# Performance work log

Hardware: AMD Instinct MI355X
Metric: run time of the kernel (lower is better)

## Reference

```python
import jax, jax.numpy as jnp
import numpy as np

B, N, K = 8, 2048, 64
RADII = (0.1, 0.3, 0.7)
TU = 256   # t_net_units
U = 512    # mmtsc_units
BLK = [(512, 512), (512, 256), (256, 170)]  # pce_depth=3, filters U//(i+1)
EPS = 1e-3  # keras BatchNormalization epsilon
BN_SCALE = np.float32(1.0 / np.sqrt(1.0 + EPS))  # inference BN: mean=0, var=1


def bn(x, g, b):
    return x * (g * BN_SCALE) + b


def setup_inputs():
    key = jax.random.key(0)
    ks = jax.random.split(key, 32)
    r = lambda i, sh, s=0.1: jax.random.normal(ks[i], sh, dtype=jnp.float32) * s
    inp = {
        "points": jax.random.normal(ks[0], (B, N, 3), dtype=jnp.float32),
        "noise": jax.random.uniform(ks[1], (B, N, N), dtype=jnp.float32),
        "tw": r(2, (3, TU)), "tb": r(3, (TU,)),
        "tg1": 1.0 + r(4, (TU,)), "tbt1": r(5, (TU,)),
        "td1w": r(6, (TU, TU)), "td1b": r(7, (TU,)),
        "tg2": 1.0 + r(8, (TU,)), "tbt2": r(9, (TU,)),
        "td2w": r(10, (TU, 9), 0.01), "td2b": jnp.ones((9,), jnp.float32),
        "c1w": r(11, (3 * K * 3, U)), "c1b": r(12, (U,)),
        "g1": 1.0 + r(13, (U,)), "be1": r(14, (U,)),
        "rw": r(15, (U, U)), "rb": r(16, (U,)),
    }
    for i, (ci, co) in enumerate(BLK):
        j = 17 + 4 * i
        inp[f"b{i+1}w"] = r(j, (ci, co))
        inp[f"b{i+1}b"] = r(j + 1, (co,))
        inp[f"b{i+1}g"] = 1.0 + r(j + 2, (co,))
        inp[f"b{i+1}be"] = r(j + 3, (co,))
    return inp


def reference(points, noise, tw, tb, tg1, tbt1, td1w, td1b, tg2, tbt2, td2w, td2b,
              c1w, c1b, g1, be1, rw, rb,
              b1w, b1b, b1g, b1be, b2w, b2b, b2g, b2be, b3w, b3b, b3g, b3be):
    relu = jax.nn.relu
    # ---- T-Net (dropout inactive at inference) ----
    x = relu(bn(points @ tw + tb, tg1, tbt1))       # [B,N,TU] (1x1 conv)
    x = jnp.max(x, axis=1)                          # GlobalMaxPooling1D -> [B,TU]
    x = relu(bn(x @ td1w + td1b, tg2, tbt2))        # [B,TU]
    T = (x @ td2w + td2b).reshape(-1, 3, 3)         # [B,3,3]
    pts = points @ T                                # [B,N,3]
    # ---- pairwise distances + multi-scale ball query ----
    diff = pts[:, :, None, :] - pts[:, None, :, :]  # [B,N,N,3]
    d = jax.lax.stop_gradient(jnp.sqrt(jnp.sum(diff * diff, axis=-1)))  # [B,N,N]
    bidx = jnp.arange(B)[:, None, None]
    groups = []
    for rad in RADII:
        score = jnp.where(d <= rad, noise, 0.0)     # mask * uniform
        idx = jnp.argsort(-score, axis=-1)[:, :, :K]  # descending, top-K  [B,N,K]
        groups.append(pts[bidx, idx])               # gather -> [B,N,K,3]
    feats = jnp.concatenate(groups, axis=-1).reshape(B, N, 3 * K * 3)  # [B,N,576]
    # ---- MLP stack (1x1 convs) ----
    f = relu(bn(feats @ c1w + c1b, g1, be1))        # [B,N,U]
    f = f + (f @ rw + rb)                           # residual
    for w, b_, g, be in ((b1w, b1b, b1g, b1be), (b2w, b2b, b2g, b2be), (b3w, b3b, b3g, b3be)):
        f = relu(bn(f @ w + b_, g, be))
    return jnp.max(f, axis=1)                       # [B,170]
```

## Files before the change

### kernel.cpp

```cpp
#include <hip/hip_runtime.h>
#include <hip/hip_bf16.h>


#define BN_SCALE 0.99950037468777f

typedef short short8 __attribute__((ext_vector_type(8)));
typedef float floatx4 __attribute__((ext_vector_type(4)));

typedef __attribute__((address_space(1))) const short gshort;
typedef __attribute__((address_space(3))) short lshort;

#define OFF_FEATS 0
#define OFF_R1    18874368
#define OFF_W     (OFF_R1 + 16777216)
#define OFF_C1WT  (OFF_W)
#define OFF_RWT   (OFF_C1WT + 589824)
#define OFF_B1WT  (OFF_RWT + 524288)
#define OFF_B2WT  (OFF_B1WT + 524288)
#define OFF_B3WT  (OFF_B2WT + 262144)
#define OFF_PTS   (OFF_B3WT + 131072)
#define OFF_PART  (OFF_PTS + 196608)

__device__ inline short f2bf(float x) {
    __hip_bfloat16 h = __float2bfloat16(x);
    return *reinterpret_cast<short*>(&h);
}
__device__ inline float bf2f(short s) {
    return __uint_as_float(((unsigned)(unsigned short)s) << 16);
}

__global__ __launch_bounds__(256)
void init_k(const float* __restrict__ c1w, const float* __restrict__ rw,
            const float* __restrict__ b1w, const float* __restrict__ b2w,
            const float* __restrict__ b3w,
            short* __restrict__ c1wT, short* __restrict__ rwT,
            short* __restrict__ b1wT, short* __restrict__ b2wT,
            short* __restrict__ b3wT,
            const float* __restrict__ points, const float* __restrict__ tw,
            const float* __restrict__ tb, const float* __restrict__ tg1,
            const float* __restrict__ tbt1, float* __restrict__ part,
            float* __restrict__ outF, int out_n) {
    __shared__ float smem[64 * 65];
    const int bid = blockIdx.x;
    if (bid < 248) {
        float (*tile)[65] = (float(*)[65])smem;
        const float* src; short* dst; int K, N, t;
        if (bid < 72)       { src = c1w; dst = c1wT; K = 576; N = 512; t = bid; }
        else if (bid < 136) { src = rw;  dst = rwT;  K = 512; N = 512; t = bid - 72; }
        else if (bid < 200) { src = b1w; dst = b1wT; K = 512; N = 512; t = bid - 136; }
        else if (bid < 232) { src = b2w; dst = b2wT; K = 512; N = 256; t = bid - 200; }
        else                { src = b3w; dst = b3wT; K = 256; N = 170; t = bid - 232; }
        int ktiles = K >> 6;
        int k0 = (t % ktiles) * 64, n0 = (t / ktiles) * 64;
        int tx = threadIdx.x & 63, ty = threadIdx.x >> 6;
#pragma unroll
        for (int p = 0; p < 16; p++) {
            int r = p * 4 + ty;
            int n = n0 + tx;
            tile[r][tx] = (n < N) ? src[(size_t)(k0 + r) * N + n] : 0.f;
        }
        __syncthreads();
#pragma unroll
        for (int p = 0; p < 16; p++) {
            int r = p * 4 + ty;
            dst[(size_t)(n0 + r) * K + k0 + tx] = f2bf(tile[tx][r]);
        }
    } else if (bid < 312) {
        float* spts = smem;
        const int t2 = bid - 248;
        const int chunk = t2 & 7, b = t2 >> 3;
        const int u = threadIdx.x;
        const float* pb = points + ((size_t)b * 2048 + chunk * 256) * 3;
        for (int i = u; i < 768; i += 256) spts[i] = pb[i];
        const float w0 = tw[u], w1 = tw[256 + u], w2 = tw[512 + u];
        const float bi = tb[u];
        const float gs = tg1[u] * BN_SCALE, bt = tbt1[u];
        __syncthreads();
        float m = 0.f;
        for (int nn = 0; nn < 256; nn++) {
            float v = spts[nn * 3] * w0 + spts[nn * 3 + 1] * w1 +
                      spts[nn * 3 + 2] * w2 + bi;
            v = fmaxf(v * gs + bt, 0.f);
            m = fmaxf(m, v);
        }
        part[((b * 8 + chunk) << 8) + u] = m;
    } else {
        for (int i = threadIdx.x; i < out_n; i += 256) outF[i] = 0.f;
    }
}

__global__ __launch_bounds__(1024)
void tnet2_k(const float* __restrict__ points, const float* __restrict__ part,
             const float* __restrict__ td1w, const float* __restrict__ td1b,
             const float* __restrict__ tg2, const float* __restrict__ tbt2,
             const float* __restrict__ td2w, const float* __restrict__ td2b,
             float* __restrict__ pts_out) {
    __shared__ float sx[256], sp[4][256], sx2[256], sp2[9][32], sT[9];
    const int b = blockIdx.x;
    const int tid = threadIdx.x;
    if (tid < 256) {
        float m = 0.f;
#pragma unroll
        for (int c = 0; c < 8; c++) m = fmaxf(m, part[((b * 8 + c) << 8) + tid]);
        sx[tid] = m;
    }
    __syncthreads();
    {
        int t = tid & 255, g = tid >> 8;
        float s = 0.f;
#pragma unroll 8
        for (int i = 0; i < 64; i++) {
            int v = g * 64 + i;
            s += sx[v] * td1w[v * 256 + t];
        }
        sp[g][t] = s;
    }
    __syncthreads();
    if (tid < 256) {
        float s = td1b[tid] + sp[0][tid] + sp[1][tid] + sp[2][tid] + sp[3][tid];
        sx2[tid] = fmaxf(s * (tg2[tid] * BN_SCALE) + tbt2[tid], 0.f);
    }
    __syncthreads();
    if (tid < 288) {
        int j = tid / 32, vg = tid & 31;
        float s = 0.f;
#pragma unroll
        for (int i = 0; i < 8; i++) {
            int v = vg * 8 + i;
            s += sx2[v] * td2w[v * 9 + j];
        }
        sp2[j][vg] = s;
    }
    __syncthreads();
    if (tid < 9) {
        float s = td2b[tid];
        for (int vg = 0; vg < 32; vg++) s += sp2[tid][vg];
        sT[tid] = s;
    }
    __syncthreads();
    for (int n = tid; n < 2048; n += 1024) {
        size_t idx = ((size_t)b * 2048 + n) * 3;
        float p0 = points[idx], p1 = points[idx + 1], p2 = points[idx + 2];
        pts_out[idx]     = p0 * sT[0] + p1 * sT[3] + p2 * sT[6];
        pts_out[idx + 1] = p0 * sT[1] + p1 * sT[4] + p2 * sT[7];
        pts_out[idx + 2] = p0 * sT[2] + p1 * sT[5] + p2 * sT[8];
    }
}

__device__ inline unsigned dpp_shr1(unsigned v) {
    return (unsigned)__builtin_amdgcn_update_dpp(0, (int)v, 0x138 ,
                                                 0xF, 0xF, false);
}

__device__ inline void ins_one(unsigned& llo, unsigned& lhi, unsigned vlo,
                               unsigned vhi, int lane) {
    unsigned long long lv = ((unsigned long long)lhi << 32) | llo;
    unsigned long long vv = ((unsigned long long)vhi << 32) | vlo;
    unsigned long long ltm = __ballot(lv < vv);
    if (ltm) {
        int p = __builtin_ctzll(ltm);
        unsigned uplo = dpp_shr1(llo);
        unsigned uphi = dpp_shr1(lhi);
        if (lane >= p) {
            llo = (lane == p) ? vlo : uplo;
            lhi = (lane == p) ? vhi : uphi;
        }
    }
}

__device__ inline void run_q(unsigned& llo, unsigned& lhi, unsigned long long& th,
                             unsigned klo, unsigned khi, unsigned long long qual,
                             int lane) {
    do {
        int src = __builtin_ctzll(qual);
        qual &= qual - 1;
        unsigned vlo = (unsigned)__builtin_amdgcn_readlane((int)klo, src);
        unsigned vhi = (unsigned)__builtin_amdgcn_readlane((int)khi, src);
        ins_one(llo, lhi, vlo, vhi, lane);
    } while (qual);
    th = ((unsigned long long)(unsigned)__builtin_amdgcn_readlane((int)lhi, 63) << 32)
         | (unsigned)__builtin_amdgcn_readlane((int)llo, 63);
}

__device__ inline void init_radius(bool in, unsigned nb, unsigned klo, int lane,
                                   unsigned& llo, unsigned& lhi,
                                   unsigned long long& th) {
    unsigned long long inm = __ballot(in);
    int S = 64 - __builtin_popcountll(inm);
    int mbI = __builtin_amdgcn_mbcnt_hi((unsigned)(inm >> 32),
              __builtin_amdgcn_mbcnt_lo((unsigned)inm, 0));
    int mbS = lane - mbI;
    int dst = in ? (S + mbI) : mbS;
    llo = (unsigned)__builtin_amdgcn_ds_permute(dst << 2, in ? 0 : (int)klo);
    lhi = 0;
    if (inm) {
        do {
            int src = __builtin_ctzll(inm);
            inm &= inm - 1;
            unsigned vlo = (unsigned)__builtin_amdgcn_readlane((int)klo, src);
            unsigned vhi = (unsigned)__builtin_amdgcn_readlane((int)nb, src);
            ins_one(llo, lhi, vlo, vhi, lane);
        } while (inm);
    }
    th = ((unsigned long long)(unsigned)__builtin_amdgcn_readlane((int)lhi, 63) << 32)
         | (unsigned)__builtin_amdgcn_readlane((int)llo, 63);
}

__global__ __launch_bounds__(512)
void topk_feats_k(const float* __restrict__ pts, const float* __restrict__ noise,
                  short* __restrict__ feats) {
    __shared__ float sxp[2048], syp[2048], szp[2048];
    const int b = blockIdx.y;
    const int tid = threadIdx.x;
    const int lane = tid & 63;
    const int wave = tid >> 6;
    const int n = blockIdx.x * 8 + wave;
    const float* nrow = noise + ((size_t)b * 2048 + n) * 2048;
    float ncur = nrow[lane];
    float nnxt = nrow[64 + lane];
    for (int i = tid; i < 2048; i += 512) {
        size_t p = ((size_t)b * 2048 + i) * 3;
        sxp[i] = pts[p];
        syp[i] = pts[p + 1];
        szp[i] = pts[p + 2];
    }
    __syncthreads();
    const float qx = sxp[n], qy = syp[n], qz = szp[n];

    unsigned L0lo, L0hi, L1lo, L1hi, L2lo, L2hi;
    unsigned long long th0, th1, th2;
    {
        float dx = qx - sxp[lane], dy = qy - syp[lane], dz = qz - szp[lane];
        float d = sqrtf(dx * dx + dy * dy + dz * dz);
        unsigned nb = __float_as_uint(ncur);
        unsigned klo = 2047 - lane;
        init_radius(d <= 0.1f, nb, klo, lane, L0lo, L0hi, th0);
        init_radius(d <= 0.3f, nb, klo, lane, L1lo, L1hi, th1);
        init_radius(d <= 0.7f, nb, klo, lane, L2lo, L2hi, th2);
    }
    for (int base = 64; base < 2048; base += 64) {
        float cur = nnxt;
        if (base + 64 < 2048) nnxt = nrow[base + 64 + lane];
        const int j = base + lane;
        float dx = qx - sxp[j], dy = qy - syp[j], dz = qz - szp[j];
        float d = sqrtf(dx * dx + dy * dy + dz * dz);
        unsigned nb = __float_as_uint(cur);
        unsigned klo = 2047 - j;
        unsigned k0hi = (d <= 0.1f) ? nb : 0u;
        unsigned k1hi = (d <= 0.3f) ? nb : 0u;
        unsigned k2hi = (d <= 0.7f) ? nb : 0u;
        unsigned long long key0 = ((unsigned long long)k0hi << 32) | klo;
        unsigned long long key1 = ((unsigned long long)k1hi << 32) | klo;
        unsigned long long key2 = ((unsigned long long)k2hi << 32) | klo;
        unsigned long long q0 = __ballot(key0 > th0);
        unsigned long long q1 = __ballot(key1 > th1);
        unsigned long long q2 = __ballot(key2 > th2);
        if (q0) run_q(L0lo, L0hi, th0, klo, k0hi, q0, lane);
        if (q1) run_q(L1lo, L1hi, th1, klo, k1hi, q1, lane);
        if (q2) run_q(L2lo, L2hi, th2, klo, k2hi, q2, lane);
    }
    size_t basef = ((size_t)b * 2048 + n) * 576 + (size_t)lane * 9;
    int j0 = 2047 - (int)(L0lo & 0x7FFu);
    int j1 = 2047 - (int)(L1lo & 0x7FFu);
    int j2 = 2047 - (int)(L2lo & 0x7FFu);
    feats[basef + 0] = f2bf(sxp[j0]);
    feats[basef + 1] = f2bf(syp[j0]);
    feats[basef + 2] = f2bf(szp[j0]);
    feats[basef + 3] = f2bf(sxp[j1]);
    feats[basef + 4] = f2bf(syp[j1]);
    feats[basef + 5] = f2bf(szp[j1]);
    feats[basef + 6] = f2bf(sxp[j2]);
    feats[basef + 7] = f2bf(syp[j2]);
    feats[basef + 8] = f2bf(szp[j2]);
}

template <int EPI>
__global__ __launch_bounds__(256)
void gemm_k(const short* __restrict__ A, const short* __restrict__ BT,
            int K, int Nact,
            const float* __restrict__ bias, const float* __restrict__ gamma,
            const float* __restrict__ beta,
            short* __restrict__ outB, float* __restrict__ outF,
            const short* __restrict__ resid) {
    __shared__ short sA[2][128 * 32];
    __shared__ short sB[2][128 * 32];
    const int tid = threadIdx.x;
    const int lane = tid & 63;
    const int wave = tid >> 6;
    const int wm = wave & 1, wn = wave >> 1;
    const int lr = lane & 15, lq = lane >> 4;
    const long m0 = (long)blockIdx.x * 128;
    const long n0 = (long)blockIdx.y * 128;

    const int srow = (lane >> 2);
    const int sp8 = (lane & 3) * 8;

    auto stage = [&](int buf, int k0) {
#pragma unroll
        for (int c = 0; c < 2; c++) {
            int chunk = wave * 2 + c;
            int rr = chunk * 16 + srow;
            __builtin_amdgcn_global_load_lds(
                (gshort*)(A + (m0 + rr) * K + k0 + sp8),
                (lshort*)&sA[buf][chunk * 512], 16, 0, 0);
            __builtin_amdgcn_global_load_lds(
                (gshort*)(BT + (n0 + rr) * K + k0 + sp8),
                (lshort*)&sB[buf][chunk * 512], 16, 0, 0);
        }
    };

    floatx4 acc[4][4];
#pragma unroll
    for (int i = 0; i < 4; i++)
#pragma unroll
        for (int j = 0; j < 4; j++) acc[i][j] = (floatx4){0.f, 0.f, 0.f, 0.f};

    const int T = K >> 5;
    stage(0, 0);
    __syncthreads();
    int cur = 0;
    for (int t = 0; t < T; ++t) {
        if (t + 1 < T) stage(cur ^ 1, (t + 1) << 5);
        short8 af[4], bf[4];
#pragma unroll
        for (int i = 0; i < 4; i++)
            af[i] = *(const short8*)(&sA[cur][(wm * 64 + i * 16 + lr) * 32 + lq * 8]);
#pragma unroll
        for (int j = 0; j < 4; j++)
            bf[j] = *(const short8*)(&sB[cur][(wn * 64 + j * 16 + lr) * 32 + lq * 8]);
#pragma unroll
        for (int i = 0; i < 4; i++)
#pragma unroll
            for (int j = 0; j < 4; j++)
                acc[i][j] = __builtin_amdgcn_mfma_f32_16x16x32_bf16(af[i], bf[j],
                                                                    acc[i][j], 0, 0, 0);
        __syncthreads();
        cur ^= 1;
    }

#pragma unroll
    for (int j = 0; j < 4; j++) {
        long col = n0 + wn * 64 + j * 16 + lr;
        if (col >= Nact) continue;
        float bi = bias[col];
        float gs = 0.f, bt = 0.f;
        if (EPI != 1) { gs = gamma[col] * BN_SCALE; bt = beta[col]; }
        float colmax = 0.f;
#pragma unroll
        for (int i = 0; i < 4; i++) {
#pragma unroll
            for (int rg = 0; rg < 4; rg++) {
                long row = m0 + wm * 64 + i * 16 + lq * 4 + rg;
                float v = acc[i][j][rg];
                if (EPI == 1) {
                    v = v + bi + bf2f(resid[row * Nact + col]);
                    outB[row * Nact + col] = f2bf(v);
                } else {
                    v = fmaxf((v + bi) * gs + bt, 0.f);
                    if (EPI == 0) outB[row * Nact + col] = f2bf(v);
                    else colmax = fmaxf(colmax, v);
                }
            }
        }
        if (EPI == 2) {
            colmax = fmaxf(colmax, __shfl_xor(colmax, 16));
            colmax = fmaxf(colmax, __shfl_xor(colmax, 32));
            if (lq == 0) {
                int bb = (int)(m0 >> 11);
                atomicMax((unsigned int*)&outF[bb * 170 + col],
                          __float_as_uint(colmax));
            }
        }
    }
}

extern "C" void kernel_launch(void* const* d_in, const int* in_sizes, int n_in,
                              void* d_out, int out_size, void* d_ws, size_t ws_size,
                              hipStream_t stream) {
    const float* points = (const float*)d_in[0];
    const float* noise  = (const float*)d_in[1];
    const float* tw   = (const float*)d_in[2];
    const float* tb   = (const float*)d_in[3];
    const float* tg1  = (const float*)d_in[4];
    const float* tbt1 = (const float*)d_in[5];
    const float* td1w = (const float*)d_in[6];
    const float* td1b = (const float*)d_in[7];
    const float* tg2  = (const float*)d_in[8];
    const float* tbt2 = (const float*)d_in[9];
    const float* td2w = (const float*)d_in[10];
    const float* td2b = (const float*)d_in[11];
    const float* c1w  = (const float*)d_in[12];
    const float* c1b  = (const float*)d_in[13];
    const float* g1   = (const float*)d_in[14];
    const float* be1  = (const float*)d_in[15];
    const float* rw   = (const float*)d_in[16];
    const float* rb   = (const float*)d_in[17];
    const float* b1w  = (const float*)d_in[18];
    const float* b1b  = (const float*)d_in[19];
    const float* b1g  = (const float*)d_in[20];
    const float* b1be = (const float*)d_in[21];
    const float* b2w  = (const float*)d_in[22];
    const float* b2b  = (const float*)d_in[23];
    const float* b2g  = (const float*)d_in[24];
    const float* b2be = (const float*)d_in[25];
    const float* b3w  = (const float*)d_in[26];
    const float* b3b  = (const float*)d_in[27];
    const float* b3g  = (const float*)d_in[28];
    const float* b3be = (const float*)d_in[29];

    char* ws = (char*)d_ws;
    short* feats = (short*)(ws + OFF_FEATS);
    short* f1    = (short*)(ws + OFF_R1);
    short* c1wT  = (short*)(ws + OFF_C1WT);
    short* rwT   = (short*)(ws + OFF_RWT);
    short* b1wT  = (short*)(ws + OFF_B1WT);
    short* b2wT  = (short*)(ws + OFF_B2WT);
    short* b3wT  = (short*)(ws + OFF_B3WT);
    float* pts   = (float*)(ws + OFF_PTS);
    float* part  = (float*)(ws + OFF_PART);
    float* outF  = (float*)d_out;

    init_k<<<313, 256, 0, stream>>>(c1w, rw, b1w, b2w, b3w,
                                    c1wT, rwT, b1wT, b2wT, b3wT,
                                    points, tw, tb, tg1, tbt1, part,
                                    outF, out_size);
    tnet2_k<<<8, 1024, 0, stream>>>(points, part, td1w, td1b, tg2, tbt2,
                                    td2w, td2b, pts);
    topk_feats_k<<<dim3(256, 8), 512, 0, stream>>>(pts, noise, feats);

    gemm_k<0><<<dim3(128, 4), 256, 0, stream>>>(feats, c1wT, 576, 512, c1b, g1, be1,
                                                f1, nullptr, nullptr);
    gemm_k<1><<<dim3(128, 4), 256, 0, stream>>>(f1, rwT, 512, 512, rb, nullptr, nullptr,
                                                feats, nullptr, f1);
    gemm_k<0><<<dim3(128, 4), 256, 0, stream>>>(feats, b1wT, 512, 512, b1b, b1g, b1be,
                                                f1, nullptr, nullptr);
    gemm_k<0><<<dim3(128, 2), 256, 0, stream>>>(f1, b2wT, 512, 256, b2b, b2g, b2be,
                                                feats, nullptr, nullptr);
    gemm_k<2><<<dim3(128, 2), 256, 0, stream>>>(feats, b3wT, 256, 170, b3b, b3g, b3be,
                                                nullptr, outF, nullptr);
}
```

Before: 437.0 us.

## Fuse the five MLP GEMMs into one kernel with activations resident in LDS

Replaces the five separate tiled GEMM launches with one kernel. Each block owns 64 rows of points and runs all MLP layers in sequence, ping-ponging the intermediate activations between two XOR-swizzled LDS buffers instead of round-tripping them through global memory. Weight fragments are now read straight from global memory (relying on L2) rather than staged through LDS, and each wave computes a slice of output columns. This removes the intermediate global writes and reads plus the launch gaps, at the cost of 128KB of LDS per block (one block per CU) and repeated per-block weight reads.

```diff
diff --git a/kernel.cpp b/kernel.cpp
--- a/kernel.cpp
+++ b/kernel.cpp
@@ -5,14 +5,19 @@
 #define BN_SCALE 0.99950037468777f
 
 typedef short short8 __attribute__((ext_vector_type(8)));
+typedef short sh4 __attribute__((ext_vector_type(4)));
 typedef float floatx4 __attribute__((ext_vector_type(4)));
 
-typedef __attribute__((address_space(1))) const short gshort;
-typedef __attribute__((address_space(3))) short lshort;
+__device__ inline short f2bf(float x) {
+    __hip_bfloat16 h = __float2bfloat16(x);
+    return *reinterpret_cast<short*>(&h);
+}
+__device__ inline float bf2f(short s) {
+    return __uint_as_float(((unsigned)(unsigned short)s) << 16);
+}
 
 #define OFF_FEATS 0
-#define OFF_R1    18874368
-#define OFF_W     (OFF_R1 + 16777216)
+#define OFF_W     18874368
 #define OFF_C1WT  (OFF_W)
 #define OFF_RWT   (OFF_C1WT + 589824)
 #define OFF_B1WT  (OFF_RWT + 524288)
@@ -20,14 +25,6 @@
 #define OFF_B3WT  (OFF_B2WT + 262144)
 #define OFF_PTS   (OFF_B3WT + 131072)
 #define OFF_PART  (OFF_PTS + 196608)
-
-__device__ inline short f2bf(float x) {
-    __hip_bfloat16 h = __float2bfloat16(x);
-    return *reinterpret_cast<short*>(&h);
-}
-__device__ inline float bf2f(short s) {
-    return __uint_as_float(((unsigned)(unsigned short)s) << 16);
-}
 
 __global__ __launch_bounds__(256)
 void init_k(const float* __restrict__ c1w, const float* __restrict__ rw,
@@ -274,104 +271,148 @@
     feats[basef + 8] = f2bf(szp[j2]);
 }
 
-template <int EPI>
-__global__ __launch_bounds__(256)
-void gemm_k(const short* __restrict__ A, const short* __restrict__ BT,
-            int K, int Nact,
-            const float* __restrict__ bias, const float* __restrict__ gamma,
-            const float* __restrict__ beta,
-            short* __restrict__ outB, float* __restrict__ outF,
-            const short* __restrict__ resid) {
-    __shared__ short sA[2][128 * 32];
-    __shared__ short sB[2][128 * 32];
+template <int NF, int EPI, int BSRC, int K>
+__device__ __forceinline__ void layer(
+    const short* __restrict__ WT, const short* __restrict__ gfeats,
+    const short* actIn, short* actOut,
+    const float* __restrict__ bias, const float* __restrict__ gamma,
+    const float* __restrict__ beta, float* __restrict__ outF,
+    int m0, int Nact) {
     const int tid = threadIdx.x;
     const int lane = tid & 63;
     const int wave = tid >> 6;
-    const int wm = wave & 1, wn = wave >> 1;
     const int lr = lane & 15, lq = lane >> 4;
-    const long m0 = (long)blockIdx.x * 128;
-    const long n0 = (long)blockIdx.y * 128;
-
-    const int srow = (lane >> 2);
-    const int sp8 = (lane & 3) * 8;
-
-    auto stage = [&](int buf, int k0) {
-#pragma unroll
-        for (int c = 0; c < 2; c++) {
-            int chunk = wave * 2 + c;
-            int rr = chunk * 16 + srow;
-            __builtin_amdgcn_global_load_lds(
-                (gshort*)(A + (m0 + rr) * K + k0 + sp8),
-                (lshort*)&sA[buf][chunk * 512], 16, 0, 0);
-            __builtin_amdgcn_global_load_lds(
-                (gshort*)(BT + (n0 + rr) * K + k0 + sp8),
-                (lshort*)&sB[buf][chunk * 512], 16, 0, 0);
-        }
-    };
-
-    floatx4 acc[4][4];
-#pragma unroll
-    for (int i = 0; i < 4; i++)
+    const int n0w = wave * (NF * 16);
+
+    floatx4 acc[NF][4];
+#pragma unroll
+    for (int i = 0; i < NF; i++)
 #pragma unroll
         for (int j = 0; j < 4; j++) acc[i][j] = (floatx4){0.f, 0.f, 0.f, 0.f};
 
-    const int T = K >> 5;
-    stage(0, 0);
-    __syncthreads();
-    int cur = 0;
-    for (int t = 0; t < T; ++t) {
-        if (t + 1 < T) stage(cur ^ 1, (t + 1) << 5);
-        short8 af[4], bf[4];
-#pragma unroll
-        for (int i = 0; i < 4; i++)
-            af[i] = *(const short8*)(&sA[cur][(wm * 64 + i * 16 + lr) * 32 + lq * 8]);
-#pragma unroll
-        for (int j = 0; j < 4; j++)
-            bf[j] = *(const short8*)(&sB[cur][(wn * 64 + j * 16 + lr) * 32 + lq * 8]);
-#pragma unroll
-        for (int i = 0; i < 4; i++)
+#pragma unroll 2
+    for (int k0 = 0; k0 < K; k0 += 32) {
+        short8 af[NF], bf[4];
+#pragma unroll
+        for (int i = 0; i < NF; i++)
+            af[i] = *(const short8*)(WT + (size_t)(n0w + i * 16 + lr) * K + k0 + lq * 8);
+        if (BSRC == 0) {
+#pragma unroll
+            for (int j = 0; j < 4; j++)
+                bf[j] = *(const short8*)(gfeats + (size_t)(m0 + j * 16 + lr) * 576 + k0 + lq * 8);
+        } else {
+#pragma unroll
+            for (int j = 0; j < 4; j++) {
+                int m = j * 16 + lr;
+                bf[j] = *(const short8*)((const char*)actIn + m * 1024 +
+                                         ((k0 * 2 + lq * 16) ^ ((m & 7) << 4)));
+            }
+        }
+#pragma unroll
+        for (int i = 0; i < NF; i++)
 #pragma unroll
             for (int j = 0; j < 4; j++)
                 acc[i][j] = __builtin_amdgcn_mfma_f32_16x16x32_bf16(af[i], bf[j],
                                                                     acc[i][j], 0, 0, 0);
-        __syncthreads();
-        cur ^= 1;
-    }
-
-#pragma unroll
-    for (int j = 0; j < 4; j++) {
-        long col = n0 + wn * 64 + j * 16 + lr;
-        if (col >= Nact) continue;
-        float bi = bias[col];
-        float gs = 0.f, bt = 0.f;
-        if (EPI != 1) { gs = gamma[col] * BN_SCALE; bt = beta[col]; }
-        float colmax = 0.f;
-#pragma unroll
-        for (int i = 0; i < 4; i++) {
+    }
+
+    if (EPI == 2) {
+        const int bb = m0 >> 11;
+#pragma unroll
+        for (int i = 0; i < NF; i++) {
+            int nb = n0w + i * 16 + lq * 4;
+            float bi[4], gs[4], bt[4], cm[4];
 #pragma unroll
             for (int rg = 0; rg < 4; rg++) {
-                long row = m0 + wm * 64 + i * 16 + lq * 4 + rg;
-                float v = acc[i][j][rg];
+                int n = nb + rg;
+                bool ok = n < Nact;
+                bi[rg] = ok ? bias[n] : 0.f;
+                gs[rg] = ok ? gamma[n] * BN_SCALE : 0.f;
+                bt[rg] = ok ? beta[n] : 0.f;
+                cm[rg] = 0.f;
+            }
+#pragma unroll
+            for (int j = 0; j < 4; j++)
+#pragma unroll
+                for (int rg = 0; rg < 4; rg++) {
+                    float v = fmaxf((acc[i][j][rg] + bi[rg]) * gs[rg] + bt[rg], 0.f);
+                    cm[rg] = fmaxf(cm[rg], v);
+                }
+#pragma unroll
+            for (int rg = 0; rg < 4; rg++) {
+                cm[rg] = fmaxf(cm[rg], __shfl_xor(cm[rg], 1));
+                cm[rg] = fmaxf(cm[rg], __shfl_xor(cm[rg], 2));
+                cm[rg] = fmaxf(cm[rg], __shfl_xor(cm[rg], 4));
+                cm[rg] = fmaxf(cm[rg], __shfl_xor(cm[rg], 8));
+            }
+            if (lr == 0) {
+#pragma unroll
+                for (int rg = 0; rg < 4; rg++) {
+                    int n = nb + rg;
+                    if (n < Nact)
+                        atomicMax((unsigned*)&outF[bb * 170 + n],
+                                  __float_as_uint(cm[rg]));
+                }
+            }
+        }
+    } else {
+#pragma unroll
+        for (int i = 0; i < NF; i++) {
+            int nb = n0w + i * 16 + lq * 4;
+            floatx4 bi = *(const floatx4*)(bias + nb);
+            floatx4 gs = {0.f, 0.f, 0.f, 0.f}, bt = {0.f, 0.f, 0.f, 0.f};
+            if (EPI == 0) {
+                gs = *(const floatx4*)(gamma + nb);
+                bt = *(const floatx4*)(beta + nb);
+            }
+#pragma unroll
+            for (int j = 0; j < 4; j++) {
+                int m = j * 16 + lr;
+                int off = m * 1024 + ((nb * 2) ^ ((m & 7) << 4));
+                sh4 pk;
                 if (EPI == 1) {
-                    v = v + bi + bf2f(resid[row * Nact + col]);
-                    outB[row * Nact + col] = f2bf(v);
+                    sh4 rs = *(const sh4*)((const char*)actIn + off);
+#pragma unroll
+                    for (int rg = 0; rg < 4; rg++)
+                        pk[rg] = f2bf(acc[i][j][rg] + bi[rg] + bf2f(rs[rg]));
                 } else {
-                    v = fmaxf((v + bi) * gs + bt, 0.f);
-                    if (EPI == 0) outB[row * Nact + col] = f2bf(v);
-                    else colmax = fmaxf(colmax, v);
+#pragma unroll
+                    for (int rg = 0; rg < 4; rg++)
+                        pk[rg] = f2bf(fmaxf((acc[i][j][rg] + bi[rg]) *
+                                            (gs[rg] * BN_SCALE) + bt[rg], 0.f));
                 }
-            }
-        }
-        if (EPI == 2) {
-            colmax = fmaxf(colmax, __shfl_xor(colmax, 16));
-            colmax = fmaxf(colmax, __shfl_xor(colmax, 32));
-            if (lq == 0) {
-                int bb = (int)(m0 >> 11);
-                atomicMax((unsigned int*)&outF[bb * 170 + col],
-                          __float_as_uint(colmax));
-            }
-        }
-    }
+                *(sh4*)((char*)actOut + off) = pk;
+            }
+        }
+    }
+}
+
+__global__ __launch_bounds__(256, 1)
+void mlp_k(const short* __restrict__ feats,
+           const short* __restrict__ c1wT, const short* __restrict__ rwT,
+           const short* __restrict__ b1wT, const short* __restrict__ b2wT,
+           const short* __restrict__ b3wT,
+           const float* __restrict__ c1b, const float* __restrict__ g1,
+           const float* __restrict__ be1, const float* __restrict__ rb,
+           const float* __restrict__ b1b, const float* __restrict__ b1g,
+           const float* __restrict__ b1be,
+           const float* __restrict__ b2b, const float* __restrict__ b2g,
+           const float* __restrict__ b2be,
+           const float* __restrict__ b3b, const float* __restrict__ b3g,
+           const float* __restrict__ b3be, float* __restrict__ outF) {
+    __shared__ __align__(16) short actA[64 * 512];
+    __shared__ __align__(16) short actB[64 * 512];
+    const int m0 = blockIdx.x * 64;
+
+    layer<8, 0, 0, 576>(c1wT, feats, nullptr, actA, c1b, g1, be1, nullptr, m0, 512);
+    __syncthreads();
+    layer<8, 1, 1, 512>(rwT, nullptr, actA, actB, rb, nullptr, nullptr, nullptr, m0, 512);
+    __syncthreads();
+    layer<8, 0, 1, 512>(b1wT, nullptr, actB, actA, b1b, b1g, b1be, nullptr, m0, 512);
+    __syncthreads();
+    layer<4, 0, 1, 512>(b2wT, nullptr, actA, actB, b2b, b2g, b2be, nullptr, m0, 256);
+    __syncthreads();
+    layer<4, 2, 1, 256>(b3wT, nullptr, actB, nullptr, b3b, b3g, b3be, outF, m0, 170);
 }
 
 extern "C" void kernel_launch(void* const* d_in, const int* in_sizes, int n_in,
@@ -410,7 +451,6 @@
 
     char* ws = (char*)d_ws;
     short* feats = (short*)(ws + OFF_FEATS);
-    short* f1    = (short*)(ws + OFF_R1);
     short* c1wT  = (short*)(ws + OFF_C1WT);
     short* rwT   = (short*)(ws + OFF_RWT);
     short* b1wT  = (short*)(ws + OFF_B1WT);
@@ -427,15 +467,7 @@
     tnet2_k<<<8, 1024, 0, stream>>>(points, part, td1w, td1b, tg2, tbt2,
                                     td2w, td2b, pts);
     topk_feats_k<<<dim3(256, 8), 512, 0, stream>>>(pts, noise, feats);
-
-    gemm_k<0><<<dim3(128, 4), 256, 0, stream>>>(feats, c1wT, 576, 512, c1b, g1, be1,
-                                                f1, nullptr, nullptr);
-    gemm_k<1><<<dim3(128, 4), 256, 0, stream>>>(f1, rwT, 512, 512, rb, nullptr, nullptr,
-                                                feats, nullptr, f1);
-    gemm_k<0><<<dim3(128, 4), 256, 0, stream>>>(feats, b1wT, 512, 512, b1b, b1g, b1be,
-                                                f1, nullptr, nullptr);
-    gemm_k<0><<<dim3(128, 2), 256, 0, stream>>>(f1, b2wT, 512, 256, b2b, b2g, b2be,
-                                                feats, nullptr, nullptr);
-    gemm_k<2><<<dim3(128, 2), 256, 0, stream>>>(feats, b3wT, 256, 170, b3b, b3g, b3be,
-                                                nullptr, outF, nullptr);
-}
+    mlp_k<<<256, 256, 0, stream>>>(feats, c1wT, rwT, b1wT, b2wT, b3wT,
+                                   c1b, g1, be1, rb, b1b, b1g, b1be,
+                                   b2b, b2g, b2be, b3b, b3g, b3be, outF);
+}
```

Measured after the change: 450.4 us. 1.03x slower.
